# Kernel tuning notes

Hardware: AMD Instinct MI355X
Metric: run time of the kernel (lower is better)

## Reference

```python
import jax, jax.numpy as jnp
import numpy as np

B, L, D, HD = 4, 4096, 2048, 128

def setup_inputs() -> dict:
    key = jax.random.key(0)
    ks = jax.random.split(key, 9)
    s = 0.02  # keep logits in a sane range
    return {
        "x": jax.random.normal(ks[0], (B, L, D), jnp.float32),
        "Wq": jax.random.normal(ks[1], (D, HD), jnp.float32) * s,
        "bq": jax.random.normal(ks[2], (HD,), jnp.float32) * s,
        "Wk": jax.random.normal(ks[3], (D, HD), jnp.float32) * s,
        "bk": jax.random.normal(ks[4], (HD,), jnp.float32) * s,
        "Wv": jax.random.normal(ks[5], (D, HD), jnp.float32) * s,
        "bv": jax.random.normal(ks[6], (HD,), jnp.float32) * s,
        "Wo": jax.random.normal(ks[7], (HD, D), jnp.float32) * s,
        "bo": jax.random.normal(ks[8], (D,), jnp.float32) * s,
    }

def reference(x, Wq, bq, Wk, bk, Wv, bv, Wo, bo):
    # x: (B, L, D)
    q = x @ Wq + bq                      # (B, L, HD)
    k = x @ Wk + bk
    v = x @ Wv + bv
    hd = q.shape[-1]
    scores = jnp.einsum('bqd,bkd->bqk', q, k) / jnp.sqrt(jnp.float32(hd))
    Lq = x.shape[1]
    causal = jnp.tril(jnp.ones((Lq, Lq), dtype=bool))  # (L, L)
    scores = jnp.where(causal, scores, -jnp.inf)
    weights = jax.nn.softmax(scores, axis=-1)          # (B, L, L)
    out = jnp.einsum('bqk,bkd->bqd', weights, v)       # (B, L, HD)
    return out @ Wo + bo                               # (B, L, D)
```

## Files before the change

### kernel.cpp

```cpp
#include <hip/hip_runtime.h>

#define B_  4
#define L_  4096
#define D_  2048
#define HD_ 128
#define M_  (B_*L_)

typedef __attribute__((ext_vector_type(8))) short short8;
typedef __attribute__((ext_vector_type(4))) float f32x4;
typedef __attribute__((ext_vector_type(16))) float f32x16;
typedef __attribute__((ext_vector_type(4))) unsigned short u16x4;
typedef __attribute__((ext_vector_type(4))) unsigned int u32x4;
typedef unsigned short u16;

#define GLL16(g, l) __builtin_amdgcn_global_load_lds( \
    (const __attribute__((address_space(1))) void*)(g), \
    (__attribute__((address_space(3))) void*)(l), 16, 0, 0)

__device__ __forceinline__ u16 f2bf(float f){
  union { float f; unsigned u; } v; v.f = f;
  unsigned r = v.u + 0x7FFFu + ((v.u >> 16) & 1u);
  return (u16)(r >> 16);
}

__device__ __forceinline__ unsigned cvtpk_bf16(float a, float b){
  unsigned r;
  asm volatile("v_cvt_pk_bf16_f32 %0, %1, %2" : "=v"(r) : "v"(a), "v"(b));
  return r;
}

__global__ __launch_bounds__(256) void prep_kernel(
    const float* __restrict__ Wq, const float* __restrict__ Wk,
    const float* __restrict__ Wv, const float* __restrict__ Wo,
    u16* __restrict__ Wt_qkv, u16* __restrict__ Wt_o)
{
  __shared__ float T[64][68];
  const int tid = threadIdx.x;
  int tb = blockIdx.x;
  int mat = tb >> 6, t = tb & 63;
  const float* src; u16* dst; int Rw, Cw, rt, ct;
  if (mat < 3) {
    src = (mat==0) ? Wq : (mat==1) ? Wk : Wv;
    dst = Wt_qkv + (size_t)mat*HD_*D_;
    Rw = D_; Cw = HD_; rt = t >> 1; ct = t & 1;
  } else {
    src = Wo; dst = Wt_o;
    Rw = HD_; Cw = D_; rt = t >> 5; ct = t & 31;
  }
  int r0 = rt*64, c0 = ct*64;
  #pragma unroll
  for (int i=0;i<4;i++){
    int fid = i*256 + tid;
    int row = fid >> 4, c4 = (fid & 15) * 4;
    float4 v = *reinterpret_cast<const float4*>(src + (size_t)(r0+row)*Cw + c0 + c4);
    *reinterpret_cast<float4*>(&T[row][c4]) = v;
  }
  __syncthreads();
  #pragma unroll
  for (int i=0;i<2;i++){
    int sid = i*256 + tid;
    int crow = sid >> 3, k8 = (sid & 7) * 8;
    short8 o;
    #pragma unroll
    for (int j=0;j<8;j++) o[j] = (short)f2bf(T[k8+j][crow]);
    *reinterpret_cast<short8*>(dst + (size_t)(c0+crow)*Rw + r0 + k8) = o;
  }
}

__global__ __launch_bounds__(512, 2) void qkv_kernel(
    const float* __restrict__ x, const u16* __restrict__ Wt,
    const float* __restrict__ bq, const float* __restrict__ bk,
    const float* __restrict__ bv,
    u16* __restrict__ Q, u16* __restrict__ Kf, u16* __restrict__ Vf)
{
  const int rb = blockIdx.x;
  const int tid  = threadIdx.x;
  const int lane = tid & 63, w = tid >> 6;
  const int wr = w >> 2, wc = w & 3;
  const int l15 = lane & 15, lhi = lane >> 4;
  const int row0 = rb * 64;

  __shared__ u16 Asm[64*64];
  __shared__ u16 Bsm[384*64];

  const u16* bSrc[6]; u16* bDst[6];
  #pragma unroll
  for (int i=0;i<6;i++){
    int id = i*512 + w*64 + lane;
    int r = id >> 3, c = (id & 7) * 8;
    bSrc[i] = Wt + (size_t)r*D_ + (c ^ ((r&7)*8));
    bDst[i] = Bsm + i*4096 + w*512;
  }
  const int ar = tid >> 3, ac = (tid & 7) * 8;
  const int aoff = ar*64 + (ac ^ ((ar&7)*8));
  const float* xrow = x + (size_t)(row0+ar)*D_ + ac;

  int offA[2][2], offB[2][6];
  #pragma unroll
  for (int ks=0;ks<2;ks++){
    #pragma unroll
    for (int m=0;m<2;m++){
      int rA = wr*32 + m*16 + l15;
      offA[ks][m] = rA*64 + ((ks*32 + lhi*8) ^ ((rA&7)*8));
    }
    #pragma unroll
    for (int n=0;n<6;n++){
      int rB = wc*96 + n*16 + l15;
      offB[ks][n] = rB*64 + ((ks*32 + lhi*8) ^ ((rB&7)*8));
    }
  }

  f32x4 acc[2][6];
  f32x4 zero4 = {0.f,0.f,0.f,0.f};
  #pragma unroll
  for (int m=0;m<2;m++)
    #pragma unroll
    for (int n=0;n<6;n++) acc[m][n] = zero4;

  float4 f0 = *reinterpret_cast<const float4*>(xrow);
  float4 f1 = *reinterpret_cast<const float4*>(xrow + 4);

  for (int k0 = 0; k0 < D_; k0 += 64) {
    __syncthreads();
    {
      short8 a8;
      a8[0]=(short)f2bf(f0.x); a8[1]=(short)f2bf(f0.y);
      a8[2]=(short)f2bf(f0.z); a8[3]=(short)f2bf(f0.w);
      a8[4]=(short)f2bf(f1.x); a8[5]=(short)f2bf(f1.y);
      a8[6]=(short)f2bf(f1.z); a8[7]=(short)f2bf(f1.w);
      *reinterpret_cast<short8*>(Asm + aoff) = a8;
    }
    #pragma unroll
    for (int i=0;i<6;i++){ GLL16(bSrc[i], bDst[i]); bSrc[i] += 64; }
    __syncthreads();
    if (k0 + 64 < D_) {
      const float* xp = xrow + k0 + 64;
      f0 = *reinterpret_cast<const float4*>(xp);
      f1 = *reinterpret_cast<const float4*>(xp + 4);
    }
    #pragma unroll
    for (int ks=0;ks<2;ks++){
      short8 fa[2], fb[6];
      #pragma unroll
      for (int m=0;m<2;m++) fa[m] = *reinterpret_cast<const short8*>(Asm + offA[ks][m]);
      #pragma unroll
      for (int n=0;n<6;n++) fb[n] = *reinterpret_cast<const short8*>(Bsm + offB[ks][n]);
      #pragma unroll
      for (int m=0;m<2;m++)
        #pragma unroll
        for (int n=0;n<6;n++)
          acc[m][n] = __builtin_amdgcn_mfma_f32_16x16x32_bf16(fa[m], fb[n], acc[m][n], 0, 0, 0);
    }
  }

  const float qscale = 0.08838834764831845f;
  #pragma unroll
  for (int n=0;n<6;n++){
    int col = wc*96 + n*16 + l15;
    int j = col >> 7;
    int c = col & 127;
    float bi = (j==0) ? bq[c] : (j==1) ? bk[c] : bv[c];
    #pragma unroll
    for (int m=0;m<2;m++){
      int rowb = row0 + wr*32 + m*16 + (lhi<<2);
      int bb = rowb >> 12;
      int l0 = rowb & (L_-1);
      if (j == 0) {
        #pragma unroll
        for (int r=0;r<4;r++)
          Q[(size_t)(rowb+r)*HD_ + c] = f2bf((acc[m][n][r] + bi) * qscale);
      } else if (j == 1) {
        int ksd = c >> 4, hid = (c >> 3) & 1, jd = c & 7;
        #pragma unroll
        for (int r=0;r<4;r++){
          int l = l0 + r;
          int kt = l >> 6, k6 = l & 63;
          int n2 = k6 >> 5, l31k = k6 & 31;
          Kf[((size_t)bb*64 + kt)*8192 + (n2*8 + ksd)*512 + (hid*32 + l31k)*8 + jd]
              = f2bf(acc[m][n][r] + bi);
        }
      } else {
        int nbv = (c >> 5) & 3, l31v = c & 31;
        int kt = l0 >> 6, k6 = l0 & 63;
        int ksv = k6 >> 4, hiv = (k6 >> 3) & 1, j0 = k6 & 7;
        u16x4 v4;
        #pragma unroll
        for (int r=0;r<4;r++) v4[r] = f2bf(acc[m][n][r] + bi);
        *reinterpret_cast<u16x4*>(
            Vf + ((size_t)bb*64 + kt)*8192 + (ksv*4 + nbv)*512 + (hiv*32 + l31v)*8 + j0) = v4;
      }
    }
  }
}

__global__ __launch_bounds__(256, 2) void attn_kernel(
    const u16* __restrict__ Qg, const u16* __restrict__ Kfg,
    const u16* __restrict__ Vfg, u16* __restrict__ AO)
{
  const int blk = blockIdx.x;
  const int xcd = blk & 7;
  const int sub = blk >> 3;
  const int b   = xcd >> 1;
  const int strip = 127 - (2*sub + (xcd & 1));
  const int q0  = strip * 32;
  const int KT  = (strip >> 1) + 1;

  const int tid = threadIdx.x, lane = tid & 63, w = tid >> 6;
  const int l31 = lane & 31;
  const int hi  = lane >> 5;

  const u16* Qb  = Qg  + (size_t)b * L_ * HD_;
  const u16* Kfb = Kfg + (size_t)b * 64 * 8192 + lane*8;
  const u16* Vfb = Vfg + (size_t)b * 64 * 8192 + lane*8;

  __shared__ __attribute__((aligned(16))) float Ol[4][32][132];
  __shared__ float Ml[4][32], Ll[4][32];

  short8 qf[8];
  #pragma unroll
  for (int ks=0; ks<8; ks++)
    qf[ks] = *reinterpret_cast<const short8*>(
        &Qb[(size_t)(q0 + l31)*HD_ + ks*16 + hi*8]);

  f32x16 O[4];
  #pragma unroll
  for (int nb=0; nb<4; nb++)
    #pragma unroll
    for (int i=0;i<16;i++) O[nb][i] = 0.f;
  float m_ = -__builtin_inff();
  float l_ = 0.f;

  for (int kt = w; kt < KT; kt += 4) {
    const u16* Kt = Kfb + (size_t)kt*8192;
    f32x16 s[2];
    #pragma unroll
    for (int n=0;n<2;n++)
      #pragma unroll
      for (int i=0;i<16;i++) s[n][i] = 0.f;
    __builtin_amdgcn_s_setprio(1);
    #pragma unroll
    for (int ks=0;ks<8;ks++)
      #pragma unroll
      for (int n=0;n<2;n++){
        short8 ka = *reinterpret_cast<const short8*>(Kt + (n*8 + ks)*512);
        s[n] = __builtin_amdgcn_mfma_f32_32x32x16_bf16(ka, qf[ks], s[n], 0, 0, 0);
      }
    __builtin_amdgcn_s_setprio(0);

    if (kt == KT-1) {
      #pragma unroll
      for (int n=0;n<2;n++)
        #pragma unroll
        for (int reg=0;reg<16;reg++){
          int key = kt*64 + n*32 + (reg&3) + 8*(reg>>2) + 4*hi;
          if (key > q0 + l31) s[n][reg] = -__builtin_inff();
        }
    }

    float pmax = s[0][0];
    #pragma unroll
    for (int n=0;n<2;n++)
      #pragma unroll
      for (int reg=0;reg<16;reg++) pmax = fmaxf(pmax, s[n][reg]);
    pmax = fmaxf(pmax, __shfl_xor(pmax, 32, 64));

    if (!__all(pmax <= m_ + 8.f)) {
      float mnew = fmaxf(m_, pmax);
      float alpha = __expf(m_ - mnew);
      m_ = mnew;
      l_ *= alpha;
      #pragma unroll
      for (int nb=0; nb<4; nb++)
        #pragma unroll
        for (int i=0;i<16;i++) O[nb][i] *= alpha;
    }

    float rsum = 0.f;
    #pragma unroll
    for (int n=0;n<2;n++)
      #pragma unroll
      for (int reg=0;reg<16;reg++){
        float p = __expf(s[n][reg] - m_);
        s[n][reg] = p;
        rsum += p;
      }
    rsum += __shfl_xor(rsum, 32, 64);
    l_ += rsum;

    unsigned c[2][8], ox[2][8];
    #pragma unroll
    for (int n=0;n<2;n++)
      #pragma unroll
      for (int i=0;i<8;i++)
        c[n][i] = cvtpk_bf16(s[n][2*i], s[n][2*i+1]);
    #pragma unroll
    for (int n=0;n<2;n++)
      #pragma unroll
      for (int i=0;i<8;i++)
        ox[n][i] = (unsigned)__shfl_xor((int)c[n][i], 32, 64);

    short8 pb[4];
    #pragma unroll
    for (int n=0;n<2;n++)
      #pragma unroll
      for (int sB=0;sB<2;sB++){
        union { u32x4 u; short8 s8; } t;
        t.u[0] = hi ? ox[n][4*sB+2] : c[n][4*sB+0];
        t.u[1] = hi ? ox[n][4*sB+3] : c[n][4*sB+1];
        t.u[2] = hi ? c[n][4*sB+2]  : ox[n][4*sB+0];
        t.u[3] = hi ? c[n][4*sB+3]  : ox[n][4*sB+1];
        pb[2*n+sB] = t.s8;
      }

    const u16* Vt2 = Vfb + (size_t)kt*8192;
    __builtin_amdgcn_s_setprio(1);
    #pragma unroll
    for (int ks=0; ks<4; ks++){
      #pragma unroll
      for (int nb=0; nb<4; nb++){
        short8 av = *reinterpret_cast<const short8*>(Vt2 + (ks*4 + nb)*512);
        O[nb] = __builtin_amdgcn_mfma_f32_32x32x16_bf16(av, pb[ks], O[nb], 0, 0, 0);
      }
    }
    __builtin_amdgcn_s_setprio(0);
  }

  if (hi == 0) { Ml[w][l31] = m_; Ll[w][l31] = l_; }
  #pragma unroll
  for (int nb=0; nb<4; nb++)
    #pragma unroll
    for (int g=0; g<4; g++){
      f32x4 v;
      v[0]=O[nb][4*g+0]; v[1]=O[nb][4*g+1]; v[2]=O[nb][4*g+2]; v[3]=O[nb][4*g+3];
      *reinterpret_cast<f32x4*>(&Ol[w][l31][nb*32 + g*8 + hi*4]) = v;
    }
  __syncthreads();

  {
    int q  = tid >> 3;
    int dc = (tid & 7) * 16;
    float mw[4], lw[4];
    float M = -__builtin_inff();
    #pragma unroll
    for (int w2=0; w2<4; w2++){ mw[w2]=Ml[w2][q]; lw[w2]=Ll[w2][q]; M = fmaxf(M, mw[w2]); }
    float den = 0.f, cw[4];
    #pragma unroll
    for (int w2=0; w2<4; w2++){ float e = __expf(mw[w2]-M); cw[w2]=e; den += lw[w2]*e; }
    float inv = 1.0f/den;
    float o[16];
    #pragma unroll
    for (int j=0;j<16;j++) o[j] = 0.f;
    #pragma unroll
    for (int w2=0; w2<4; w2++){
      #pragma unroll
      for (int g=0; g<4; g++){
        f32x4 p = *reinterpret_cast<const f32x4*>(&Ol[w2][q][dc + g*4]);
        #pragma unroll
        for (int j=0;j<4;j++) o[g*4+j] += cw[w2]*p[j];
      }
    }
    short8 st0, st1;
    #pragma unroll
    for (int j=0;j<8;j++){ st0[j] = (short)f2bf(o[j]*inv); st1[j] = (short)f2bf(o[8+j]*inv); }
    u16* dst = &AO[((size_t)b*L_ + q0 + q)*HD_ + dc];
    *reinterpret_cast<short8*>(dst)     = st0;
    *reinterpret_cast<short8*>(dst + 8) = st1;
  }
}

__global__ __launch_bounds__(256) void proj_kernel(
    const u16* __restrict__ AO, const u16* __restrict__ Wt_o,
    const float* __restrict__ bo, float* __restrict__ out)
{
  const int nb = blockIdx.x;
  const int rb = blockIdx.y;
  const int tid = threadIdx.x, lane = tid & 63, w = tid >> 6;
  const int wr = w >> 1, wc = w & 1;
  const int l15 = lane & 15, lhi = lane >> 4;
  const int row0 = rb * 128, n0 = nb * 128;

  __shared__ u16 Al[128][136];
  __shared__ u16 Bl[128][136];

  #pragma unroll
  for (int i=0;i<8;i++){
    int chunk = i*256 + tid;
    int r = chunk >> 4;
    int c = (chunk & 15) * 8;
    *reinterpret_cast<short8*>(&Al[r][c]) =
        *reinterpret_cast<const short8*>(&AO[(size_t)(row0+r)*HD_ + c]);
    *reinterpret_cast<short8*>(&Bl[r][c]) =
        *reinterpret_cast<const short8*>(&Wt_o[(size_t)(n0+r)*HD_ + c]);
  }
  __syncthreads();

  f32x4 acc[4][4];
  f32x4 zero4 = {0.f,0.f,0.f,0.f};
  for (int m=0;m<4;m++) for (int n=0;n<4;n++) acc[m][n] = zero4;

  #pragma unroll
  for (int ks=0; ks<128; ks+=32){
    short8 fa[4], fb[4];
    #pragma unroll
    for (int m=0;m<4;m++)
      fa[m] = *reinterpret_cast<const short8*>(&Al[wr*64 + m*16 + l15][ks + (lhi<<3)]);
    #pragma unroll
    for (int n=0;n<4;n++)
      fb[n] = *reinterpret_cast<const short8*>(&Bl[wc*64 + n*16 + l15][ks + (lhi<<3)]);
    #pragma unroll
    for (int m=0;m<4;m++)
      #pragma unroll
      for (int n=0;n<4;n++)
        acc[m][n] = __builtin_amdgcn_mfma_f32_16x16x32_bf16(fa[m], fb[n], acc[m][n], 0, 0, 0);
  }

  #pragma unroll
  for (int n=0;n<4;n++){
    int col = n0 + wc*64 + n*16 + l15;
    float b = bo[col];
    #pragma unroll
    for (int m=0;m<4;m++){
      #pragma unroll
      for (int r=0;r<4;r++){
        int row = row0 + wr*64 + m*16 + (lhi<<2) + r;
        out[(size_t)row*D_ + col] = acc[m][n][r] + b;
      }
    }
  }
}

extern "C" void kernel_launch(void* const* d_in, const int* in_sizes, int n_in,
                              void* d_out, int out_size, void* d_ws, size_t ws_size,
                              hipStream_t stream) {
  const float* x  = (const float*)d_in[0];
  const float* Wq = (const float*)d_in[1];
  const float* bq = (const float*)d_in[2];
  const float* Wk = (const float*)d_in[3];
  const float* bk = (const float*)d_in[4];
  const float* Wv = (const float*)d_in[5];
  const float* bv = (const float*)d_in[6];
  const float* Wo = (const float*)d_in[7];
  const float* bo = (const float*)d_in[8];
  float* out = (float*)d_out;

  u16* ws      = (u16*)d_ws;
  u16* Wt_qkv  = ws;
  u16* Wt_o    = Wt_qkv + 3*HD_*D_;
  u16* Q       = Wt_o   + (size_t)D_*HD_;
  u16* Kf      = Q + (size_t)M_*HD_;
  u16* Vf      = Kf + (size_t)M_*HD_;
  u16* AO      = Vf + (size_t)M_*HD_;

  prep_kernel<<<256, 256, 0, stream>>>(Wq, Wk, Wv, Wo, Wt_qkv, Wt_o);
  qkv_kernel<<<256, 512, 0, stream>>>(x, Wt_qkv, bq, bk, bv, Q, Kf, Vf);
  attn_kernel<<<512, 256, 0, stream>>>(Q, Kf, Vf, AO);
  proj_kernel<<<dim3(16, 128), 256, 0, stream>>>(AO, Wt_o, bo, out);
}
```

Measured before the change: 169.1 us.

## Double-buffer QKV projection shared-memory tiles to overlap loads with MFMA

Converts the QKV projection GEMM main loop to use two LDS buffers for the x and W tiles. The next W tile is issued with global_load_lds and the x tile is prefetched two steps ahead while the current tile is being multiplied. This cuts the loop from two barriers per k-step to one and hides global load latency. In exchange, shared memory per block roughly doubles (about 112KB), which may limit the intended two blocks per CU and lower occupancy.

```diff
diff --git a/kernel.cpp b/kernel.cpp
--- a/kernel.cpp
+++ b/kernel.cpp
@@ -80,16 +80,16 @@
   const int l15 = lane & 15, lhi = lane >> 4;
   const int row0 = rb * 64;
 
-  __shared__ u16 Asm[64*64];
-  __shared__ u16 Bsm[384*64];
-
-  const u16* bSrc[6]; u16* bDst[6];
+  __shared__ u16 Asm[2][64*64];
+  __shared__ u16 Bsm[2][384*64];
+
+  const u16* bSrc[6]; int bDstOff[6];
   #pragma unroll
   for (int i=0;i<6;i++){
     int id = i*512 + w*64 + lane;
     int r = id >> 3, c = (id & 7) * 8;
     bSrc[i] = Wt + (size_t)r*D_ + (c ^ ((r&7)*8));
-    bDst[i] = Bsm + i*4096 + w*512;
+    bDstOff[i] = i*4096 + w*512;
   }
   const int ar = tid >> 3, ac = (tid & 7) * 8;
   const int aoff = ar*64 + (ac ^ ((ar&7)*8));
@@ -117,40 +117,60 @@
     #pragma unroll
     for (int n=0;n<6;n++) acc[m][n] = zero4;
 
-  float4 f0 = *reinterpret_cast<const float4*>(xrow);
-  float4 f1 = *reinterpret_cast<const float4*>(xrow + 4);
-
-  for (int k0 = 0; k0 < D_; k0 += 64) {
-    __syncthreads();
-    {
-      short8 a8;
-      a8[0]=(short)f2bf(f0.x); a8[1]=(short)f2bf(f0.y);
-      a8[2]=(short)f2bf(f0.z); a8[3]=(short)f2bf(f0.w);
-      a8[4]=(short)f2bf(f1.x); a8[5]=(short)f2bf(f1.y);
-      a8[6]=(short)f2bf(f1.z); a8[7]=(short)f2bf(f1.w);
-      *reinterpret_cast<short8*>(Asm + aoff) = a8;
-    }
-    #pragma unroll
-    for (int i=0;i<6;i++){ GLL16(bSrc[i], bDst[i]); bSrc[i] += 64; }
-    __syncthreads();
-    if (k0 + 64 < D_) {
-      const float* xp = xrow + k0 + 64;
-      f0 = *reinterpret_cast<const float4*>(xp);
-      f1 = *reinterpret_cast<const float4*>(xp + 4);
-    }
+  float4 xa0 = *reinterpret_cast<const float4*>(xrow);
+  float4 xa1 = *reinterpret_cast<const float4*>(xrow + 4);
+  #pragma unroll
+  for (int i=0;i<6;i++){ GLL16(bSrc[i], &Bsm[0][bDstOff[i]]); bSrc[i] += 64; }
+  {
+    short8 a8;
+    a8[0]=(short)f2bf(xa0.x); a8[1]=(short)f2bf(xa0.y);
+    a8[2]=(short)f2bf(xa0.z); a8[3]=(short)f2bf(xa0.w);
+    a8[4]=(short)f2bf(xa1.x); a8[5]=(short)f2bf(xa1.y);
+    a8[6]=(short)f2bf(xa1.z); a8[7]=(short)f2bf(xa1.w);
+    *reinterpret_cast<short8*>(&Asm[0][aoff]) = a8;
+  }
+  xa0 = *reinterpret_cast<const float4*>(xrow + 64);
+  xa1 = *reinterpret_cast<const float4*>(xrow + 68);
+  __syncthreads();
+
+  for (int t = 0; t < 32; ++t) {
+    const int cur = t & 1, nxt = cur ^ 1;
+    const bool more = (t + 1 < 32);
+    float4 xb0, xb1;
+    if (t + 2 < 32) {
+      const float* xp = xrow + (t+2)*64;
+      xb0 = *reinterpret_cast<const float4*>(xp);
+      xb1 = *reinterpret_cast<const float4*>(xp + 4);
+    }
+    if (more) {
+      #pragma unroll
+      for (int i=0;i<6;i++){ GLL16(bSrc[i], &Bsm[nxt][bDstOff[i]]); bSrc[i] += 64; }
+    }
+    const u16* Ac = &Asm[cur][0];
+    const u16* Bc = &Bsm[cur][0];
     #pragma unroll
     for (int ks=0;ks<2;ks++){
       short8 fa[2], fb[6];
       #pragma unroll
-      for (int m=0;m<2;m++) fa[m] = *reinterpret_cast<const short8*>(Asm + offA[ks][m]);
-      #pragma unroll
-      for (int n=0;n<6;n++) fb[n] = *reinterpret_cast<const short8*>(Bsm + offB[ks][n]);
+      for (int m=0;m<2;m++) fa[m] = *reinterpret_cast<const short8*>(Ac + offA[ks][m]);
+      #pragma unroll
+      for (int n=0;n<6;n++) fb[n] = *reinterpret_cast<const short8*>(Bc + offB[ks][n]);
       #pragma unroll
       for (int m=0;m<2;m++)
         #pragma unroll
         for (int n=0;n<6;n++)
           acc[m][n] = __builtin_amdgcn_mfma_f32_16x16x32_bf16(fa[m], fb[n], acc[m][n], 0, 0, 0);
     }
+    if (more) {
+      short8 a8;
+      a8[0]=(short)f2bf(xa0.x); a8[1]=(short)f2bf(xa0.y);
+      a8[2]=(short)f2bf(xa0.z); a8[3]=(short)f2bf(xa0.w);
+      a8[4]=(short)f2bf(xa1.x); a8[5]=(short)f2bf(xa1.y);
+      a8[6]=(short)f2bf(xa1.z); a8[7]=(short)f2bf(xa1.w);
+      *reinterpret_cast<short8*>(&Asm[nxt][aoff]) = a8;
+    }
+    __syncthreads();
+    xa0 = xb0; xa1 = xb1;
   }
 
   const float qscale = 0.08838834764831845f;
```

New measurement: 158.3 us. -6.4%, faster.

## Pre-swizzle weights and attention output into MFMA fragment layout, drop LDS staging

Applied to the files above, without the earlier changes.

The weight prep kernel now writes Wqkv and Wo directly in per-lane MFMA fragment order, and the attention kernel writes its output in the same fragment order. The QKV GEMM then loads B fragments straight from global memory instead of staging them in LDS. It double-buffers fp32 x tiles via global_load_lds and converts them to bf16 with packed cvt at fragment-load time, using 32-row blocks with 256 threads. The projection kernel drops LDS entirely and reads fragments directly. This removes LDS traffic and barriers, at the cost of more global and L2 traffic for the weights and smaller tiles with less reuse.

```diff
diff --git a/kernel.cpp b/kernel.cpp
--- a/kernel.cpp
+++ b/kernel.cpp
@@ -32,20 +32,19 @@
 __global__ __launch_bounds__(256) void prep_kernel(
     const float* __restrict__ Wq, const float* __restrict__ Wk,
     const float* __restrict__ Wv, const float* __restrict__ Wo,
-    u16* __restrict__ Wt_qkv, u16* __restrict__ Wt_o)
+    u16* __restrict__ Wf_qkv, u16* __restrict__ Wf_o)
 {
   __shared__ float T[64][68];
   const int tid = threadIdx.x;
   int tb = blockIdx.x;
-  int mat = tb >> 6, t = tb & 63;
-  const float* src; u16* dst; int Rw, Cw, rt, ct;
+  int mat = tb >> 6, tt = tb & 63;
+  const float* src; int Rw, Cw, rt, ct;
   if (mat < 3) {
     src = (mat==0) ? Wq : (mat==1) ? Wk : Wv;
-    dst = Wt_qkv + (size_t)mat*HD_*D_;
-    Rw = D_; Cw = HD_; rt = t >> 1; ct = t & 1;
+    Rw = D_; Cw = HD_; rt = tt >> 1; ct = tt & 1;
   } else {
-    src = Wo; dst = Wt_o;
-    Rw = HD_; Cw = D_; rt = t >> 5; ct = t & 31;
+    src = Wo;
+    Rw = HD_; Cw = D_; rt = tt >> 5; ct = tt & 31;
   }
   int r0 = rt*64, c0 = ct*64;
   #pragma unroll
@@ -63,12 +62,25 @@
     short8 o;
     #pragma unroll
     for (int j=0;j<8;j++) o[j] = (short)f2bf(T[k8+j][crow]);
-    *reinterpret_cast<short8*>(dst + (size_t)(c0+crow)*Rw + r0 + k8) = o;
-  }
-}
-
-__global__ __launch_bounds__(512, 2) void qkv_kernel(
-    const float* __restrict__ x, const u16* __restrict__ Wt,
+    int K = r0 + k8;
+    if (mat < 3) {
+      int C = mat*128 + c0 + crow;
+      int t2 = K >> 6, ks = (K >> 5) & 1, lh = (K >> 3) & 3;
+      int g = C >> 4, l15c = C & 15;
+      size_t off = ((size_t)((t2*2 + ks)*24 + g)*64 + (lh*16 + l15c))*8;
+      *reinterpret_cast<short8*>(Wf_qkv + off) = o;
+    } else {
+      int C = c0 + crow;
+      int ks = K >> 5, lh = (K >> 3) & 3;
+      int g = C >> 4, l15c = C & 15;
+      size_t off = ((size_t)(ks*128 + g)*64 + (lh*16 + l15c))*8;
+      *reinterpret_cast<short8*>(Wf_o + off) = o;
+    }
+  }
+}
+
+__global__ __launch_bounds__(256, 2) void qkv_kernel(
+    const float* __restrict__ x, const u16* __restrict__ Wf,
     const float* __restrict__ bq, const float* __restrict__ bk,
     const float* __restrict__ bv,
     u16* __restrict__ Q, u16* __restrict__ Kf, u16* __restrict__ Vf)
@@ -76,39 +88,28 @@
   const int rb = blockIdx.x;
   const int tid  = threadIdx.x;
   const int lane = tid & 63, w = tid >> 6;
-  const int wr = w >> 2, wc = w & 3;
   const int l15 = lane & 15, lhi = lane >> 4;
-  const int row0 = rb * 64;
-
-  __shared__ u16 Asm[64*64];
-  __shared__ u16 Bsm[384*64];
-
-  const u16* bSrc[6]; u16* bDst[6];
-  #pragma unroll
-  for (int i=0;i<6;i++){
-    int id = i*512 + w*64 + lane;
-    int r = id >> 3, c = (id & 7) * 8;
-    bSrc[i] = Wt + (size_t)r*D_ + (c ^ ((r&7)*8));
-    bDst[i] = Bsm + i*4096 + w*512;
-  }
-  const int ar = tid >> 3, ac = (tid & 7) * 8;
-  const int aoff = ar*64 + (ac ^ ((ar&7)*8));
-  const float* xrow = x + (size_t)(row0+ar)*D_ + ac;
-
-  int offA[2][2], offB[2][6];
-  #pragma unroll
-  for (int ks=0;ks<2;ks++){
-    #pragma unroll
-    for (int m=0;m<2;m++){
-      int rA = wr*32 + m*16 + l15;
-      offA[ks][m] = rA*64 + ((ks*32 + lhi*8) ^ ((rA&7)*8));
-    }
-    #pragma unroll
-    for (int n=0;n<6;n++){
-      int rB = wc*96 + n*16 + l15;
-      offB[ks][n] = rB*64 + ((ks*32 + lhi*8) ^ ((rB&7)*8));
-    }
-  }
+  const int row0 = rb * 32;
+
+  __shared__ float Asm[2][32*64];
+
+  const float* aSrc[2]; 
+  #pragma unroll
+  for (int i=0;i<2;i++){
+    int c = w*2 + i;
+    int row = c*4 + (lane >> 4);
+    int k4  = (lane & 15) * 4;
+    int ksrc = k4 ^ ((row & 7) << 3);
+    aSrc[i] = x + (size_t)(row0 + row)*D_ + ksrc;
+  }
+  int offA[2][2];
+  #pragma unroll
+  for (int ks=0;ks<2;ks++)
+    #pragma unroll
+    for (int m=0;m<2;m++)
+      offA[ks][m] = (m*16 + l15)*64 + ((ks*32 + lhi*8) ^ ((l15 & 7) << 3));
+
+  const u16* wfLane = Wf + lane*8;
 
   f32x4 acc[2][6];
   f32x4 zero4 = {0.f,0.f,0.f,0.f};
@@ -117,52 +118,61 @@
     #pragma unroll
     for (int n=0;n<6;n++) acc[m][n] = zero4;
 
-  float4 f0 = *reinterpret_cast<const float4*>(xrow);
-  float4 f1 = *reinterpret_cast<const float4*>(xrow + 4);
-
-  for (int k0 = 0; k0 < D_; k0 += 64) {
-    __syncthreads();
-    {
-      short8 a8;
-      a8[0]=(short)f2bf(f0.x); a8[1]=(short)f2bf(f0.y);
-      a8[2]=(short)f2bf(f0.z); a8[3]=(short)f2bf(f0.w);
-      a8[4]=(short)f2bf(f1.x); a8[5]=(short)f2bf(f1.y);
-      a8[6]=(short)f2bf(f1.z); a8[7]=(short)f2bf(f1.w);
-      *reinterpret_cast<short8*>(Asm + aoff) = a8;
-    }
-    #pragma unroll
-    for (int i=0;i<6;i++){ GLL16(bSrc[i], bDst[i]); bSrc[i] += 64; }
-    __syncthreads();
-    if (k0 + 64 < D_) {
-      const float* xp = xrow + k0 + 64;
-      f0 = *reinterpret_cast<const float4*>(xp);
-      f1 = *reinterpret_cast<const float4*>(xp + 4);
-    }
+  #pragma unroll
+  for (int i=0;i<2;i++){
+    GLL16(aSrc[i], &Asm[0][(w*2+i)*256]);
+    aSrc[i] += 64;
+  }
+  __syncthreads();
+
+  for (int t = 0; t < 32; ++t) {
+    const int cur = t & 1;
+    if (t + 1 < 32) {
+      #pragma unroll
+      for (int i=0;i<2;i++){
+        GLL16(aSrc[i], &Asm[cur^1][(w*2+i)*256]);
+        aSrc[i] += 64;
+      }
+    }
+    const float* Ac = &Asm[cur][0];
     #pragma unroll
     for (int ks=0;ks<2;ks++){
-      short8 fa[2], fb[6];
-      #pragma unroll
-      for (int m=0;m<2;m++) fa[m] = *reinterpret_cast<const short8*>(Asm + offA[ks][m]);
-      #pragma unroll
-      for (int n=0;n<6;n++) fb[n] = *reinterpret_cast<const short8*>(Bsm + offB[ks][n]);
+      short8 fb[6];
+      const u16* fbp = wfLane + (size_t)((t*2 + ks)*24 + w*6)*512;
+      #pragma unroll
+      for (int n=0;n<6;n++)
+        fb[n] = *reinterpret_cast<const short8*>(fbp + n*512);
+      short8 fa[2];
+      #pragma unroll
+      for (int m=0;m<2;m++){
+        float4 f0 = *reinterpret_cast<const float4*>(Ac + offA[ks][m]);
+        float4 f1 = *reinterpret_cast<const float4*>(Ac + offA[ks][m] + 4);
+        union { u32x4 u; short8 s8; } tt;
+        tt.u[0] = cvtpk_bf16(f0.x, f0.y);
+        tt.u[1] = cvtpk_bf16(f0.z, f0.w);
+        tt.u[2] = cvtpk_bf16(f1.x, f1.y);
+        tt.u[3] = cvtpk_bf16(f1.z, f1.w);
+        fa[m] = tt.s8;
+      }
       #pragma unroll
       for (int m=0;m<2;m++)
         #pragma unroll
         for (int n=0;n<6;n++)
           acc[m][n] = __builtin_amdgcn_mfma_f32_16x16x32_bf16(fa[m], fb[n], acc[m][n], 0, 0, 0);
     }
+    __syncthreads();
   }
 
   const float qscale = 0.08838834764831845f;
   #pragma unroll
   for (int n=0;n<6;n++){
-    int col = wc*96 + n*16 + l15;
+    int col = w*96 + n*16 + l15;
     int j = col >> 7;
     int c = col & 127;
     float bi = (j==0) ? bq[c] : (j==1) ? bk[c] : bv[c];
     #pragma unroll
     for (int m=0;m<2;m++){
-      int rowb = row0 + wr*32 + m*16 + (lhi<<2);
+      int rowb = row0 + m*16 + (lhi<<2);
       int bb = rowb >> 12;
       int l0 = rowb & (L_-1);
       if (j == 0) {
@@ -195,7 +205,7 @@
 
 __global__ __launch_bounds__(256, 2) void attn_kernel(
     const u16* __restrict__ Qg, const u16* __restrict__ Kfg,
-    const u16* __restrict__ Vfg, u16* __restrict__ AO)
+    const u16* __restrict__ Vfg, u16* __restrict__ AOf)
 {
   const int blk = blockIdx.x;
   const int xcd = blk & 7;
@@ -362,53 +372,48 @@
     short8 st0, st1;
     #pragma unroll
     for (int j=0;j<8;j++){ st0[j] = (short)f2bf(o[j]*inv); st1[j] = (short)f2bf(o[8+j]*inv); }
-    u16* dst = &AO[((size_t)b*L_ + q0 + q)*HD_ + dc];
-    *reinterpret_cast<short8*>(dst)     = st0;
-    *reinterpret_cast<short8*>(dst + 8) = st1;
+    size_t rowg = (size_t)b*L_ + q0 + q;
+    size_t rb2g = rowg >> 5;
+    int qq = (int)(rowg & 31);
+    int mA = qq >> 4, l15A = qq & 15;
+    int ks0 = dc >> 5,      lh0 = (dc >> 3) & 3;
+    int ks1 = (dc+8) >> 5,  lh1 = ((dc+8) >> 3) & 3;
+    *reinterpret_cast<short8*>(AOf + ((rb2g*4 + ks0)*2 + mA)*512 + (lh0*16 + l15A)*8) = st0;
+    *reinterpret_cast<short8*>(AOf + ((rb2g*4 + ks1)*2 + mA)*512 + (lh1*16 + l15A)*8) = st1;
   }
 }
 
 __global__ __launch_bounds__(256) void proj_kernel(
-    const u16* __restrict__ AO, const u16* __restrict__ Wt_o,
+    const u16* __restrict__ AOf, const u16* __restrict__ Wf_o,
     const float* __restrict__ bo, float* __restrict__ out)
 {
-  const int nb = blockIdx.x;
-  const int rb = blockIdx.y;
+  const int nb  = blockIdx.x;
+  const int rbk = blockIdx.y;
   const int tid = threadIdx.x, lane = tid & 63, w = tid >> 6;
-  const int wr = w >> 1, wc = w & 1;
   const int l15 = lane & 15, lhi = lane >> 4;
-  const int row0 = rb * 128, n0 = nb * 128;
-
-  __shared__ u16 Al[128][136];
-  __shared__ u16 Bl[128][136];
-
-  #pragma unroll
-  for (int i=0;i<8;i++){
-    int chunk = i*256 + tid;
-    int r = chunk >> 4;
-    int c = (chunk & 15) * 8;
-    *reinterpret_cast<short8*>(&Al[r][c]) =
-        *reinterpret_cast<const short8*>(&AO[(size_t)(row0+r)*HD_ + c]);
-    *reinterpret_cast<short8*>(&Bl[r][c]) =
-        *reinterpret_cast<const short8*>(&Wt_o[(size_t)(n0+r)*HD_ + c]);
-  }
-  __syncthreads();
-
-  f32x4 acc[4][4];
+
+  const u16* faBase = AOf  + (size_t)rbk*8*512 + lane*8;
+  const u16* fbBase = Wf_o + lane*8;
+
+  f32x4 acc[2][4];
   f32x4 zero4 = {0.f,0.f,0.f,0.f};
-  for (int m=0;m<4;m++) for (int n=0;n<4;n++) acc[m][n] = zero4;
-
-  #pragma unroll
-  for (int ks=0; ks<128; ks+=32){
-    short8 fa[4], fb[4];
-    #pragma unroll
-    for (int m=0;m<4;m++)
-      fa[m] = *reinterpret_cast<const short8*>(&Al[wr*64 + m*16 + l15][ks + (lhi<<3)]);
+  #pragma unroll
+  for (int m=0;m<2;m++)
+    #pragma unroll
+    for (int n=0;n<4;n++) acc[m][n] = zero4;
+
+  #pragma unroll
+  for (int ks=0; ks<4; ks++){
+    short8 fa[2], fb[4];
+    #pragma unroll
+    for (int m=0;m<2;m++)
+      fa[m] = *reinterpret_cast<const short8*>(faBase + (ks*2 + m)*512);
     #pragma unroll
     for (int n=0;n<4;n++)
-      fb[n] = *reinterpret_cast<const short8*>(&Bl[wc*64 + n*16 + l15][ks + (lhi<<3)]);
-    #pragma unroll
-    for (int m=0;m<4;m++)
+      fb[n] = *reinterpret_cast<const short8*>(
+          fbBase + (size_t)(ks*128 + nb*16 + w*4 + n)*512);
+    #pragma unroll
+    for (int m=0;m<2;m++)
       #pragma unroll
       for (int n=0;n<4;n++)
         acc[m][n] = __builtin_amdgcn_mfma_f32_16x16x32_bf16(fa[m], fb[n], acc[m][n], 0, 0, 0);
@@ -416,15 +421,14 @@
 
   #pragma unroll
   for (int n=0;n<4;n++){
-    int col = n0 + wc*64 + n*16 + l15;
-    float b = bo[col];
-    #pragma unroll
-    for (int m=0;m<4;m++){
-      #pragma unroll
-      for (int r=0;r<4;r++){
-        int row = row0 + wr*64 + m*16 + (lhi<<2) + r;
-        out[(size_t)row*D_ + col] = acc[m][n][r] + b;
-      }
+    int col = nb*256 + w*64 + n*16 + l15;
+    float bi = bo[col];
+    #pragma unroll
+    for (int m=0;m<2;m++){
+      int row = rbk*32 + m*16 + (lhi<<2);
+      #pragma unroll
+      for (int r=0;r<4;r++)
+        out[(size_t)(row+r)*D_ + col] = acc[m][n][r] + bi;
     }
   }
 }
@@ -444,15 +448,15 @@
   float* out = (float*)d_out;
 
   u16* ws      = (u16*)d_ws;
-  u16* Wt_qkv  = ws;
-  u16* Wt_o    = Wt_qkv + 3*HD_*D_;
-  u16* Q       = Wt_o   + (size_t)D_*HD_;
+  u16* Wf_qkv  = ws;
+  u16* Wf_o    = Wf_qkv + 3*HD_*D_;
+  u16* Q       = Wf_o   + (size_t)D_*HD_;
   u16* Kf      = Q + (size_t)M_*HD_;
   u16* Vf      = Kf + (size_t)M_*HD_;
-  u16* AO      = Vf + (size_t)M_*HD_;
-
-  prep_kernel<<<256, 256, 0, stream>>>(Wq, Wk, Wv, Wo, Wt_qkv, Wt_o);
-  qkv_kernel<<<256, 512, 0, stream>>>(x, Wt_qkv, bq, bk, bv, Q, Kf, Vf);
-  attn_kernel<<<512, 256, 0, stream>>>(Q, Kf, Vf, AO);
-  proj_kernel<<<dim3(16, 128), 256, 0, stream>>>(AO, Wt_o, bo, out);
-}
+  u16* AOf     = Vf + (size_t)M_*HD_;
+
+  prep_kernel<<<256, 256, 0, stream>>>(Wq, Wk, Wv, Wo, Wf_qkv, Wf_o);
+  qkv_kernel<<<512, 256, 0, stream>>>(x, Wf_qkv, bq, bk, bv, Q, Kf, Vf);
+  attn_kernel<<<512, 256, 0, stream>>>(Q, Kf, Vf, AOf);
+  proj_kernel<<<dim3(8, 512), 256, 0, stream>>>(AOf, Wf_o, bo, out);
+}
```

Result: slower. 174.1 us, median of 2 (+3.0%).
